# Performance work log

Hardware: AMD Instinct MI355X
Metric: run time of the kernel (lower is better)

## Reference

```python
import jax, jax.numpy as jnp
import numpy as np

HEADS = 64
HEAD_DIM = 4
C = 256
T = 32  # num_ds_tokens
MAX_Q_CHUNK = 256


def conv1x1(x, W, b):
    # x: (N,C,H,W), W: (O,C), b: (O,)
    return jnp.einsum('oc,nchw->nohw', W, x) + b[None, :, None, None]


def reshape_heads(x):
    n, c, h, w = x.shape
    return x.reshape(n, HEADS, HEAD_DIM, h * w)


def chunked_attention(q, k, v, ds_token_count, chunk):
    # q: (N,h,d,L); k,v: (N,h,d,M)
    N, H, D, L = q.shape
    scale = 1.0 / float(np.sqrt(D))
    nc = L // chunk
    qs = q.reshape(N, H, D, nc, chunk).transpose(3, 0, 1, 2, 4)  # (nc,N,h,d,chunk)

    def body(carry, qc):
        logits = jnp.einsum('nhdl,nhdm->nhlm', qc, k) * scale
        w = jax.nn.softmax(logits, axis=-1)
        out = jnp.einsum('nhlm,nhdm->nhdl', w, v)
        total = jnp.clip(w.sum(axis=-1, keepdims=True), 1e-6, None)
        dsr = w[..., -ds_token_count:].sum(axis=-1, keepdims=True) / total  # (N,h,chunk,1)
        return carry, (out, dsr)

    _, (outs, dsrs) = jax.lax.scan(body, None, qs)
    attn_out = outs.transpose(1, 2, 3, 0, 4).reshape(N, H, D, L)
    ds_ratio_mean = dsrs.mean(axis=(0, 2, 3, 4))  # mean over heads, tokens -> (N,)
    return attn_out, ds_ratio_mean


def forward(spatials, invs, dss, Wq, bq, Wk, bk, Wv, bv, Wo, bo, Wdsk, bdsk, Wdsv, bdsv, ds_gate):
    fused_feats = []
    ds_ratios = []
    for i in range(4):
        sp, inv, ds = spatials[i], invs[i], dss[i]
        N, c, Hh, Ww = sp.shape
        q = reshape_heads(conv1x1(sp, Wq[i], bq[i]))
        k_sp = reshape_heads(conv1x1(inv, Wk[i], bk[i]))
        v_sp = reshape_heads(conv1x1(inv, Wv[i], bv[i]))
        pooled = ds.mean(axis=(2, 3))  # (N,C)
        key_tok = (pooled @ Wdsk[i].T + bdsk[i]).reshape(N, HEADS, HEAD_DIM, T)
        val_tok = (pooled @ Wdsv[i].T + bdsv[i]).reshape(N, HEADS, HEAD_DIM, T)
        gate = jax.nn.sigmoid(ds_gate[i])
        val_tok = val_tok * gate
        k = jnp.concatenate([k_sp, key_tok], axis=-1)
        v = jnp.concatenate([v_sp, val_tok], axis=-1)
        L = Hh * Ww
        chunk = min(MAX_Q_CHUNK, L)
        attn_out, dsr = chunked_attention(q, k, v, T, chunk)
        attn_out = attn_out.reshape(N, C, Hh, Ww)
        fused = sp + conv1x1(attn_out, Wo[i], bo[i])
        fused_feats.append(fused)
        ds_ratios.append(dsr)
    return (*fused_feats, jnp.stack(ds_ratios))


def setup_inputs() -> dict:
    key = jax.random.key(0)
    ks = jax.random.split(key, 32)
    sizes = [64, 32, 16, 8]
    inp = {}
    j = 0
    for pref in ('s', 'i', 'd'):
        for lvl, hw in enumerate(sizes):
            inp[f'{pref}{lvl}'] = jax.random.normal(ks[j], (2, C, hw, hw), dtype=jnp.float32)
            j += 1
    w = 0.02
    inp['Wq'] = jax.random.normal(ks[j], (4, C, C), dtype=jnp.float32) * w; j += 1
    inp['bq'] = jnp.zeros((4, C), dtype=jnp.float32)
    inp['Wk'] = jax.random.normal(ks[j], (4, C, C), dtype=jnp.float32) * w; j += 1
    inp['bk'] = jnp.zeros((4, C), dtype=jnp.float32)
    inp['Wv'] = jax.random.normal(ks[j], (4, C, C), dtype=jnp.float32) * w; j += 1
    inp['bv'] = jnp.zeros((4, C), dtype=jnp.float32)
    inp['Wo'] = jax.random.normal(ks[j], (4, C, C), dtype=jnp.float32) * w; j += 1
    inp['bo'] = jnp.zeros((4, C), dtype=jnp.float32)
    inp['Wdsk'] = jax.random.normal(ks[j], (4, HEADS * HEAD_DIM * T, C), dtype=jnp.float32) * w; j += 1
    inp['bdsk'] = jnp.zeros((4, HEADS * HEAD_DIM * T), dtype=jnp.float32)
    inp['Wdsv'] = jax.random.normal(ks[j], (4, HEADS * HEAD_DIM * T, C), dtype=jnp.float32) * w; j += 1
    inp['bdsv'] = jnp.zeros((4, HEADS * HEAD_DIM * T), dtype=jnp.float32)
    inp['ds_gate'] = jnp.zeros((4,), dtype=jnp.float32)
    return inp


def reference(s0, s1, s2, s3, i0, i1, i2, i3, d0, d1, d2, d3,
              Wq, bq, Wk, bk, Wv, bv, Wo, bo, Wdsk, bdsk, Wdsv, bdsv, ds_gate):
    return forward((s0, s1, s2, s3), (i0, i1, i2, i3), (d0, d1, d2, d3),
                   Wq, bq, Wk, bk, Wv, bv, Wo, bo, Wdsk, bdsk, Wdsv, bdsv, ds_gate)
```

## Files before the change

kernel.cpp:

```cpp
#include <hip/hip_runtime.h>
#include <math.h>

#define CCH 256
#define NB 2
#define HEADS 64
#define QK_SCALE (0.72134752f * 1024.0f)
#define SCH_MAGIC 15316.0f

typedef _Float16 f16;
typedef _Float16 f16x8 __attribute__((ext_vector_type(8)));
typedef _Float16 f16x4 __attribute__((ext_vector_type(4)));
typedef float f32x4 __attribute__((ext_vector_type(4)));

static const size_t OFF_POOLED = 0;
static const size_t OFF_DSACC  = 2048;
static const size_t H_Q   = 0;
static const size_t H_K   = 2785280;
static const size_t H_V   = 5636096;
static const size_t H_ATT = 8486912;
static const size_t H_SPT = 11272192;
static const size_t H_IVT = 14057472;
static const size_t H_W   = 16842752;

static const size_t DS_OUT_OFF = 2785280;

__device__ __forceinline__ void lvl_tables(int lvl, int& L, int& M, size_t& qo, size_t& kvo) {
    const int Ls[4] = {4096, 1024, 256, 64};
    const size_t qoff[4] = {0, 2097152, 2621440, 2752512};
    const size_t kvoff[4] = {0, 2113536, 2654208, 2801664};
    L = Ls[lvl]; M = L + 32; qo = qoff[lvl]; kvo = kvoff[lvl];
}

struct P12 { const float* a[12]; };

__global__ __launch_bounds__(256)
void prep_kernel(P12 ptrs, const float* __restrict__ Wq, const float* __restrict__ Wk,
                 const float* __restrict__ Wv, const float* __restrict__ Wo,
                 f16* __restrict__ WF, f16* __restrict__ spT, f16* __restrict__ ivT,
                 float* __restrict__ pooled, float* __restrict__ dsacc) {
    int id = blockIdx.x;
    if (id < 5440) {
        __shared__ float tile[32][33];
        int x = id % 170, rest = id / 170;
        int y = rest & 7, z = rest >> 3;
        int lvl, xl;
        if (x < 128) { lvl = 0; xl = x; }
        else if (x < 160) { lvl = 1; xl = x - 128; }
        else if (x < 168) { lvl = 2; xl = x - 160; }
        else { lvl = 3; xl = x - 168; }
        int L, M; size_t qo, kvo;
        lvl_tables(lvl, L, M, qo, kvo);
        int src = z >> 1, n = z & 1;
        const float* X = ptrs.a[src * 4 + lvl];
        f16* XT = (src == 0 ? spT : ivT) + qo;
        int c0 = y * 32, l0 = xl * 32;
        int tx = threadIdx.x & 31, ty = threadIdx.x >> 5;
        #pragma unroll
        for (int k = 0; k < 4; k++) {
            int c = c0 + ty + k * 8;
            tile[ty + k * 8][tx] = X[((size_t)n * CCH + c) * L + l0 + tx];
        }
        __syncthreads();
        #pragma unroll
        for (int k = 0; k < 4; k++) {
            int l = l0 + ty + k * 8;
            XT[((size_t)n * L + l) * CCH + c0 + tx] = (f16)tile[tx][ty + k * 8];
        }
    } else if (id < 6464) {
        int wI = id - 5440;
        int x = wI & 255, setId = wI >> 8;
        const float* src = (setId == 0) ? Wq : (setId == 1) ? Wk : (setId == 2) ? Wv : Wo;
        size_t i = ((size_t)x * 256 + threadIdx.x) * 4;
        float4 v = *(const float4*)(src + i);
        f16x4 o;
        o[0] = (f16)v.x; o[1] = (f16)v.y; o[2] = (f16)v.z; o[3] = (f16)v.w;
        *(f16x4*)(WF + (size_t)setId * 262144 + i) = o;
    } else {
        if (id == 6464) {
            dsacc[threadIdx.x] = 0.f;
            dsacc[threadIdx.x + 256] = 0.f;
        }
        int lin = (id - 6464) * 4 + (threadIdx.x >> 6);
        int c = lin & 255, n = (lin >> 8) & 1, lvl = lin >> 9;
        int t = threadIdx.x & 63;
        const float* d = ptrs.a[8 + lvl];
        int L = 4096 >> (2 * lvl);
        const float* p = d + ((size_t)n * CCH + c) * L;
        float s = 0.f;
        for (int i = t; i < L; i += 64) s += p[i];
        #pragma unroll
        for (int off = 32; off > 0; off >>= 1) s += __shfl_down(s, off);
        if (t == 0) pooled[(lvl * NB + n) * CCH + c] = s / (float)L;
    }
}

__global__ __launch_bounds__(256)
void mid_kernel(const f16* __restrict__ spT, const f16* __restrict__ ivT,
                const f16* __restrict__ WF,
                const float* __restrict__ bq, const float* __restrict__ bk,
                const float* __restrict__ bv,
                f16* __restrict__ qF, f16* __restrict__ kF, f16* __restrict__ vF,
                const float* __restrict__ Wdsk, const float* __restrict__ bdsk,
                const float* __restrict__ Wdsv, const float* __restrict__ bdsv,
                const float* __restrict__ ds_gate, const float* __restrict__ pooled) {
    int id = blockIdx.x;
    if (id >= 1032) {
        int dI = id - 1032;
        int bx = dI & 63, lvl = dI >> 6;
        int t = threadIdx.x;
        int j = bx * 128 + (t >> 1);
        int half = t & 1;
        const float4* wk = (const float4*)(Wdsk + ((size_t)lvl * 8192 + j) * CCH) + half * 32;
        const float4* wv = (const float4*)(Wdsv + ((size_t)lvl * 8192 + j) * CCH) + half * 32;
        const float4* p0 = (const float4*)(pooled + (size_t)(lvl * NB + 0) * CCH) + half * 32;
        const float4* p1 = (const float4*)(pooled + (size_t)(lvl * NB + 1) * CCH) + half * 32;
        float ak0 = 0.f, ak1 = 0.f, av0 = 0.f, av1 = 0.f;
        #pragma unroll 8
        for (int c4 = 0; c4 < 32; c4++) {
            float4 a = wk[c4], b = wv[c4], pa = p0[c4], pb = p1[c4];
            ak0 += a.x * pa.x + a.y * pa.y + a.z * pa.z + a.w * pa.w;
            ak1 += a.x * pb.x + a.y * pb.y + a.z * pb.z + a.w * pb.w;
            av0 += b.x * pa.x + b.y * pa.y + b.z * pa.z + b.w * pa.w;
            av1 += b.x * pb.x + b.y * pb.y + b.z * pb.z + b.w * pb.w;
        }
        ak0 += __shfl_xor(ak0, 1); ak1 += __shfl_xor(ak1, 1);
        av0 += __shfl_xor(av0, 1); av1 += __shfl_xor(av1, 1);
        if (half) return;
        float bk_ = bdsk[lvl * 8192 + j], bv_ = bdsv[lvl * 8192 + j];
        float gate = 1.f / (1.f + __expf(-ds_gate[lvl]));
        ak0 += bk_; ak1 += bk_;
        av0 = (av0 + bv_) * gate; av1 = (av1 + bv_) * gate;
        int o = j >> 5, tk = j & 31;
        int L, M; size_t qo, kvo;
        lvl_tables(lvl, L, M, qo, kvo);
        int hh = o >> 2, dd = o & 3;
        kF[kvo + ((size_t)(0 * 64 + hh)) * (4 * (size_t)M) + (size_t)(L + tk) * 4 + dd] = (f16)ak0;
        kF[kvo + ((size_t)(1 * 64 + hh)) * (4 * (size_t)M) + (size_t)(L + tk) * 4 + dd] = (f16)ak1;
        vF[kvo + ((size_t)(0 * 64 + hh)) * (4 * (size_t)M) + (size_t)dd * M + (L + tk)] = (f16)av0;
        vF[kvo + ((size_t)(1 * 64 + hh)) * (4 * (size_t)M) + (size_t)dd * M + (L + tk)] = (f16)av1;
        return;
    }
    int x = id % 43, rest = id / 43;
    int yb = rest % 12, n = rest / 12;
    int lvl, xl;
    if (x < 32) { lvl = 0; xl = x; }
    else if (x < 40) { lvl = 1; xl = x - 32; }
    else if (x < 42) { lvl = 2; xl = x - 40; }
    else { lvl = 3; xl = x - 42; }
    int L, M; size_t qo, kvo;
    lvl_tables(lvl, L, M, qo, kvo);
    const int type = yb >> 2;
    const int ob = (yb & 3) * 64;
    const int t = threadIdx.x, w = t >> 6, lane = t & 63;
    const int quad = lane >> 4, n16 = lane & 15;
    const int l0w = xl * 128 + w * 32;
    if (l0w >= L) return;

    const f16* XT = ((type == 0) ? spT : ivT) + qo;
    const f16* Wf = WF + (size_t)type * 262144 + (size_t)lvl * 65536;
    const float* bias = ((type == 0) ? bq : (type == 1) ? bk : bv) + lvl * 256;

    f32x4 acc[4][2];
    #pragma unroll
    for (int f = 0; f < 4; f++)
        #pragma unroll
        for (int g = 0; g < 2; g++) { acc[f][g][0]=0.f; acc[f][g][1]=0.f; acc[f][g][2]=0.f; acc[f][g][3]=0.f; }

    const f16* xp = XT + ((size_t)n * L + l0w + n16) * CCH + quad * 8;
    const f16* wp = Wf + ((size_t)(ob + n16)) * CCH + quad * 8;

    #pragma unroll
    for (int c0 = 0; c0 < 256; c0 += 32) {
        f16x8 af[4], bf[2];
        #pragma unroll
        for (int f = 0; f < 4; f++) af[f] = *(const f16x8*)(wp + (size_t)f * 16 * CCH + c0);
        #pragma unroll
        for (int g = 0; g < 2; g++) bf[g] = *(const f16x8*)(xp + (size_t)g * 16 * CCH + c0);
        #pragma unroll
        for (int f = 0; f < 4; f++)
            #pragma unroll
            for (int g = 0; g < 2; g++)
                acc[f][g] = __builtin_amdgcn_mfma_f32_16x16x32_f16(af[f], bf[g], acc[f][g], 0, 0, 0);
    }

    #pragma unroll
    for (int f = 0; f < 4; f++) {
        #pragma unroll
        for (int g = 0; g < 2; g++) {
            int lloc = l0w + g * 16 + n16;
            float vals[4];
            #pragma unroll
            for (int r = 0; r < 4; r++)
                vals[r] = acc[f][g][r] + bias[ob + f * 16 + quad * 4 + r];
            if (type == 0) {
                #pragma unroll
                for (int r = 0; r < 4; r++)
                    qF[qo + ((size_t)n * CCH + ob + f * 16 + quad * 4 + r) * (size_t)L + lloc] =
                        (f16)(vals[r] * QK_SCALE);
            } else if (type == 1) {
                f16x4 pk;
                #pragma unroll
                for (int r = 0; r < 4; r++) pk[r] = (f16)vals[r];
                int hh = (ob + f * 16 + quad * 4) >> 2;
                *(f16x4*)(kF + kvo + ((size_t)(n * 64 + hh)) * (4 * (size_t)M) + (size_t)lloc * 4) = pk;
            } else {
                int hh = (ob + f * 16 + quad * 4) >> 2;
                f16* vdst = vF + kvo + ((size_t)(n * 64 + hh)) * (4 * (size_t)M) + lloc;
                #pragma unroll
                for (int r = 0; r < 4; r++)
                    vdst[(size_t)r * M] = (f16)vals[r];
            }
        }
    }
}

__global__ __launch_bounds__(256, 6)
void attn_all_kernel(const f16* __restrict__ qBase, const f16* __restrict__ kBase,
                     const f16* __restrict__ vBase, f16* __restrict__ attBase,
                     float* __restrict__ dsacc) {
    int x = blockIdx.x, lvl, xl;
    if (x < 16) { lvl = 0; xl = x; }
    else if (x < 20) { lvl = 1; xl = x - 16; }
    else if (x < 21) { lvl = 2; xl = 0; }
    else { lvl = 3; xl = 0; }
    int L, M; size_t qo, kvo;
    lvl_tables(lvl, L, M, qo, kvo);
    const f16* qb = qBase + qo;
    f16* attT = attBase + qo;

    const int h = blockIdx.y, b = blockIdx.z;
    const int t = threadIdx.x, w = t >> 6, lane = t & 63;
    const int quad = lane >> 4, n16 = lane & 15;
    const size_t qbase = ((size_t)b * CCH + h * 4) * (size_t)L;
    const int mperm = ((n16 & 12) << 1) + (n16 & 3);
    const int base_tile = xl * 16;

    const f16* kh = kBase + kvo + ((size_t)(b * 64 + h)) * (4 * (size_t)M);
    const f16* vh = vBase + kvo + ((size_t)(b * 64 + h)) * (4 * (size_t)M);
    const f16* kpm = kh + (size_t)mperm * 4;
    const f16* vpm = vh + (size_t)(n16 & 3) * M + quad * 8;
    const bool vlane = (n16 < 4);

    f16x4 qf[4];
    f32x4 acc[4];
    #pragma unroll
    for (int i = 0; i < 4; i++) {
        #pragma unroll
        for (int e = 0; e < 4; e++) qf[i][e] = (f16)0.f;
        acc[i][0] = 0.f; acc[i][1] = 0.f; acc[i][2] = 0.f; acc[i][3] = 0.f;
    }

    f32x4 magic;
    magic[0] = SCH_MAGIC; magic[1] = SCH_MAGIC; magic[2] = SCH_MAGIC; magic[3] = SCH_MAGIC;

    f16x8 vcon0, vconL;
    {
        f16 c0 = (f16)((n16 == 4) ? 1.f : 0.f);
        f16 cL = (f16)((n16 == 4 || n16 == 5) ? 1.f : 0.f);
        #pragma unroll
        for (int e = 0; e < 8; e++) { vcon0[e] = c0; vconL[e] = cL; }
    }

#define LOADKV(m0_, ka_, kb_, vf_)                                                      \
    do {                                                                                \
        ka_ = *(const f16x4*)(kpm + (size_t)(m0_) * 4);                                 \
        kb_ = *(const f16x4*)(kpm + (size_t)(m0_) * 4 + 16);                            \
        vf_ = *(const f16x8*)(vpm + (m0_));                                             \
    } while (0)

#define COMPUTE32(ka_, kb_, vfl_, vcon_)                                                \
    do {                                                                                \
        f16x8 vf = vlane ? (vfl_) : (vcon_);                                            \
        f32x4 s[4][2];                                                                  \
        _Pragma("unroll")                                                               \
        for (int j = 0; j < 4; j++) {                                                   \
            s[j][0] = __builtin_amdgcn_mfma_f32_16x16x16f16((ka_), qf[j], magic, 0, 0, 0);  \
            s[j][1] = __builtin_amdgcn_mfma_f32_16x16x16f16((kb_), qf[j], magic, 0, 0, 0); \
        }                                                                               \
        _Pragma("unroll")                                                               \
        for (int j = 0; j < 4; j++) {                                                   \
            union { unsigned u[4]; f16x8 hh; } Wu;                                      \
            Wu.u[0] = ((unsigned)(int)s[j][0][0]) | (((unsigned)(int)s[j][0][1]) << 16); \
            Wu.u[1] = ((unsigned)(int)s[j][0][2]) | (((unsigned)(int)s[j][0][3]) << 16); \
            Wu.u[2] = ((unsigned)(int)s[j][1][0]) | (((unsigned)(int)s[j][1][1]) << 16); \
            Wu.u[3] = ((unsigned)(int)s[j][1][2]) | (((unsigned)(int)s[j][1][3]) << 16); \
            acc[j] = __builtin_amdgcn_mfma_f32_16x16x32_f16(Wu.hh, vf, acc[j], 0, 0, 0); \
        }                                                                               \
    } while (0)

    if (base_tile * 16 + 256 <= L) {
        if (quad == 0) {
            #pragma unroll
            for (int i = 0; i < 4; i++) {
                int l = (base_tile + i * 4 + w) * 16 + n16;
                #pragma unroll
                for (int d = 0; d < 4; d++) qf[i][d] = qb[qbase + (size_t)d * L + l];
            }
        }
        f16x4 kaA, kbA, kaB, kbB;
        f16x8 vA, vB;
        LOADKV(0, kaA, kbA, vA);
        for (int m0 = 0; m0 < L; m0 += 64) {
            LOADKV(m0 + 32, kaB, kbB, vB);
            COMPUTE32(kaA, kbA, vA, vcon0);
            LOADKV(m0 + 64, kaA, kbA, vA);
            COMPUTE32(kaB, kbB, vB, vcon0);
        }
        COMPUTE32(kaA, kbA, vA, vconL);
    } else {
        bool valid[4];
        #pragma unroll
        for (int i = 0; i < 4; i++) {
            int tl0 = (base_tile + i * 4 + w) * 16;
            valid[i] = (tl0 < L);
            if (valid[i] && quad == 0) {
                int l = tl0 + n16;
                #pragma unroll
                for (int d = 0; d < 4; d++) qf[i][d] = qb[qbase + (size_t)d * L + l];
            }
        }
        for (int m0 = 0; m0 < M; m0 += 32) {
            f16x4 ka = *(const f16x4*)(kpm + (size_t)m0 * 4);
            f16x4 kb2 = *(const f16x4*)(kpm + (size_t)m0 * 4 + 16);
            f16x8 vfl = *(const f16x8*)(vpm + m0);
            f16x8 vf = vlane ? vfl : ((m0 >= L) ? vconL : vcon0);
            f32x4 s[4][2];
            #pragma unroll
            for (int j = 0; j < 4; j++) {
                if (!valid[j]) continue;
                s[j][0] = __builtin_amdgcn_mfma_f32_16x16x16f16(ka, qf[j], magic, 0, 0, 0);
                s[j][1] = __builtin_amdgcn_mfma_f32_16x16x16f16(kb2, qf[j], magic, 0, 0, 0);
            }
            #pragma unroll
            for (int j = 0; j < 4; j++) {
                if (!valid[j]) continue;
                union { unsigned u[4]; f16x8 hh; } Wu;
                Wu.u[0] = ((unsigned)(int)s[j][0][0]) | (((unsigned)(int)s[j][0][1]) << 16);
                Wu.u[1] = ((unsigned)(int)s[j][0][2]) | (((unsigned)(int)s[j][0][3]) << 16);
                Wu.u[2] = ((unsigned)(int)s[j][1][0]) | (((unsigned)(int)s[j][1][1]) << 16);
                Wu.u[3] = ((unsigned)(int)s[j][1][2]) | (((unsigned)(int)s[j][1][3]) << 16);
                acc[j] = __builtin_amdgcn_mfma_f32_16x16x32_f16(Wu.hh, vf, acc[j], 0, 0, 0);
            }
        }
    }
#undef LOADKV
#undef COMPUTE32

    float dsr = 0.f;
    #pragma unroll
    for (int i = 0; i < 4; i++) {
        int tl0 = (base_tile + i * 4 + w) * 16;
        if (tl0 >= L) continue;
        #pragma unroll
        for (int r = 0; r < 4; r++) {
            float den = __shfl(acc[i][r], (lane & 48) | 4, 64);
            float rcp = 1.f / den;
            int l = tl0 + quad * 4 + r;
            if (n16 < 4)
                attT[((size_t)b * L + l) * CCH + h * 4 + n16] = (f16)(acc[i][r] * rcp);
            if (n16 == 5) dsr += acc[i][r] * rcp;
        }
    }
    dsr += __shfl_xor(dsr, 16, 64);
    dsr += __shfl_xor(dsr, 32, 64);
    if (n16 == 5 && quad == 0) atomicAdd(dsacc + (size_t)lvl * 128 + (size_t)b * 64 + h, dsr);
}

__global__ __launch_bounds__(256)
void convo_kernel(const f16* __restrict__ attT, const f16* __restrict__ WF,
                  const float* __restrict__ bo, const float* __restrict__ s0,
                  const float* __restrict__ s1, const float* __restrict__ s2,
                  const float* __restrict__ s3, float* __restrict__ out,
                  const float* __restrict__ dsacc) {
    if (blockIdx.x == 0 && blockIdx.y == 0 && blockIdx.z == 0 && threadIdx.x < 64) {
        int tt = threadIdx.x;
        #pragma unroll
        for (int i = 0; i < 8; i++) {
            float v = dsacc[i * 64 + tt];
            #pragma unroll
            for (int off = 32; off > 0; off >>= 1) v += __shfl_down(v, off);
            if (tt == 0) {
                int lv = i >> 1;
                out[DS_OUT_OFF + i] = v / (float)(HEADS * (4096 >> (2 * lv)));
            }
        }
    }
    int x = blockIdx.x, lvl, xl;
    if (x < 32) { lvl = 0; xl = x; }
    else if (x < 40) { lvl = 1; xl = x - 32; }
    else if (x < 42) { lvl = 2; xl = x - 40; }
    else { lvl = 3; xl = x - 42; }
    int L, M; size_t qo, kvo;
    lvl_tables(lvl, L, M, qo, kvo);
    const float* resid = (lvl == 0) ? s0 : (lvl == 1) ? s1 : (lvl == 2) ? s2 : s3;
    const int ob = blockIdx.y * 64;
    const int n = blockIdx.z;
    const int t = threadIdx.x, w = t >> 6, lane = t & 63;
    const int quad = lane >> 4, n16 = lane & 15;
    const int l0w = xl * 128 + w * 32;
    if (l0w >= L) return;

    const f16* Wf = WF + 3 * 262144 + (size_t)lvl * 65536;
    const float* bias = bo + lvl * 256;

    f32x4 acc[4][2];
    #pragma unroll
    for (int f = 0; f < 4; f++)
        #pragma unroll
        for (int g = 0; g < 2; g++) { acc[f][g][0]=0.f; acc[f][g][1]=0.f; acc[f][g][2]=0.f; acc[f][g][3]=0.f; }

    const f16* xp = attT + qo + ((size_t)n * L + l0w + n16) * CCH + quad * 8;
    const f16* wp = Wf + ((size_t)(ob + n16)) * CCH + quad * 8;

    #pragma unroll
    for (int c0 = 0; c0 < 256; c0 += 32) {
        f16x8 af[4], bf[2];
        #pragma unroll
        for (int f = 0; f < 4; f++) af[f] = *(const f16x8*)(wp + (size_t)f * 16 * CCH + c0);
        #pragma unroll
        for (int g = 0; g < 2; g++) bf[g] = *(const f16x8*)(xp + (size_t)g * 16 * CCH + c0);
        #pragma unroll
        for (int f = 0; f < 4; f++)
            #pragma unroll
            for (int g = 0; g < 2; g++)
                acc[f][g] = __builtin_amdgcn_mfma_f32_16x16x32_f16(af[f], bf[g], acc[f][g], 0, 0, 0);
    }

    #pragma unroll
    for (int f = 0; f < 4; f++) {
        #pragma unroll
        for (int g = 0; g < 2; g++) {
            int lloc = l0w + g * 16 + n16;
            #pragma unroll
            for (int r = 0; r < 4; r++) {
                size_t idx = qo + ((size_t)n * CCH + ob + f * 16 + quad * 4 + r) * (size_t)L + lloc;
                out[idx] = acc[f][g][r] + bias[ob + f * 16 + quad * 4 + r] + resid[idx - qo];
            }
        }
    }
}

extern "C" void kernel_launch(void* const* d_in, const int* in_sizes, int n_in,
                              void* d_out, int out_size, void* d_ws, size_t ws_size,
                              hipStream_t stream) {
    const float* sp[4] = {(const float*)d_in[0], (const float*)d_in[1], (const float*)d_in[2], (const float*)d_in[3]};
    const float* iv[4] = {(const float*)d_in[4], (const float*)d_in[5], (const float*)d_in[6], (const float*)d_in[7]};
    const float* dd[4] = {(const float*)d_in[8], (const float*)d_in[9], (const float*)d_in[10], (const float*)d_in[11]};
    const float* Wq = (const float*)d_in[12];
    const float* bq = (const float*)d_in[13];
    const float* Wk = (const float*)d_in[14];
    const float* bk = (const float*)d_in[15];
    const float* Wv = (const float*)d_in[16];
    const float* bv = (const float*)d_in[17];
    const float* Wo = (const float*)d_in[18];
    const float* bo = (const float*)d_in[19];
    const float* Wdsk = (const float*)d_in[20];
    const float* bdsk = (const float*)d_in[21];
    const float* Wdsv = (const float*)d_in[22];
    const float* bdsv = (const float*)d_in[23];
    const float* gate = (const float*)d_in[24];

    float* ws = (float*)d_ws;
    float* pooled = ws + OFF_POOLED;
    float* dsacc = ws + OFF_DSACC;
    f16* hb = (f16*)((char*)d_ws + 10240);
    f16* qF   = hb + H_Q;
    f16* kF   = hb + H_K;
    f16* vF   = hb + H_V;
    f16* attF = hb + H_ATT;
    f16* spT  = hb + H_SPT;
    f16* ivT  = hb + H_IVT;
    f16* WF   = hb + H_W;
    float* out = (float*)d_out;

    P12 ptrs;
    for (int i = 0; i < 4; i++) { ptrs.a[i] = sp[i]; ptrs.a[4 + i] = iv[i]; ptrs.a[8 + i] = dd[i]; }

    prep_kernel<<<dim3(6976), 256, 0, stream>>>(ptrs, Wq, Wk, Wv, Wo, WF, spT, ivT, pooled, dsacc);

    mid_kernel<<<dim3(1288), 256, 0, stream>>>(spT, ivT, WF, bq, bk, bv, qF, kF, vF,
                                               Wdsk, bdsk, Wdsv, bdsv, gate, pooled);

    attn_all_kernel<<<dim3(22, 64, 2), 256, 0, stream>>>(qF, kF, vF, attF, dsacc);

    convo_kernel<<<dim3(43, 4, 2), 256, 0, stream>>>(attF, WF, bo, sp[0], sp[1], sp[2], sp[3],
                                                     out, dsacc);
}
```

Before: 475.0 us.

## Interleave K layout for single 16-byte loads and deepen attention prefetch

Measured after the change: 900.4 us. 1.9x slower.

```diff
diff --git a/kernel.cpp b/kernel.cpp
--- a/kernel.cpp
+++ b/kernel.cpp
@@ -29,6 +29,11 @@
     const size_t qoff[4] = {0, 2097152, 2621440, 2752512};
     const size_t kvoff[4] = {0, 2113536, 2654208, 2801664};
     L = Ls[lvl]; M = L + 32; qo = qoff[lvl]; kvo = kvoff[lvl];
+}
+
+__device__ __forceinline__ size_t k_off(int l, int d) {
+    return ((size_t)(l >> 5)) * 128 + (size_t)((((l >> 3) & 3) * 4 + (l & 3)) * 8)
+         + (size_t)(((l >> 2) & 1) * 4) + (size_t)d;
 }
 
 struct P12 { const float* a[12]; };
@@ -134,8 +139,9 @@
         int L, M; size_t qo, kvo;
         lvl_tables(lvl, L, M, qo, kvo);
         int hh = o >> 2, dd = o & 3;
-        kF[kvo + ((size_t)(0 * 64 + hh)) * (4 * (size_t)M) + (size_t)(L + tk) * 4 + dd] = (f16)ak0;
-        kF[kvo + ((size_t)(1 * 64 + hh)) * (4 * (size_t)M) + (size_t)(L + tk) * 4 + dd] = (f16)ak1;
+        size_t koff = k_off(L + tk, dd);
+        kF[kvo + ((size_t)(0 * 64 + hh)) * (4 * (size_t)M) + koff] = (f16)ak0;
+        kF[kvo + ((size_t)(1 * 64 + hh)) * (4 * (size_t)M) + koff] = (f16)ak1;
         vF[kvo + ((size_t)(0 * 64 + hh)) * (4 * (size_t)M) + (size_t)dd * M + (L + tk)] = (f16)av0;
         vF[kvo + ((size_t)(1 * 64 + hh)) * (4 * (size_t)M) + (size_t)dd * M + (L + tk)] = (f16)av1;
         return;
@@ -201,8 +207,9 @@
                 f16x4 pk;
                 #pragma unroll
                 for (int r = 0; r < 4; r++) pk[r] = (f16)vals[r];
-                int hh = (ob + f * 16 + quad * 4) >> 2;
-                *(f16x4*)(kF + kvo + ((size_t)(n * 64 + hh)) * (4 * (size_t)M) + (size_t)lloc * 4) = pk;
+                int o4 = ob + f * 16 + quad * 4;
+                int hh = o4 >> 2;
+                *(f16x4*)(kF + kvo + ((size_t)(n * 64 + hh)) * (4 * (size_t)M) + k_off(lloc, 0)) = pk;
             } else {
                 int hh = (ob + f * 16 + quad * 4) >> 2;
                 f16* vdst = vF + kvo + ((size_t)(n * 64 + hh)) * (4 * (size_t)M) + lloc;
@@ -232,12 +239,11 @@
     const int t = threadIdx.x, w = t >> 6, lane = t & 63;
     const int quad = lane >> 4, n16 = lane & 15;
     const size_t qbase = ((size_t)b * CCH + h * 4) * (size_t)L;
-    const int mperm = ((n16 & 12) << 1) + (n16 & 3);
     const int base_tile = xl * 16;
 
     const f16* kh = kBase + kvo + ((size_t)(b * 64 + h)) * (4 * (size_t)M);
     const f16* vh = vBase + kvo + ((size_t)(b * 64 + h)) * (4 * (size_t)M);
-    const f16* kpm = kh + (size_t)mperm * 4;
+    const f16* kpmP = kh + n16 * 8;
     const f16* vpm = vh + (size_t)(n16 & 3) * M + quad * 8;
     const bool vlane = (n16 < 4);
 
@@ -261,21 +267,23 @@
         for (int e = 0; e < 8; e++) { vcon0[e] = c0; vconL[e] = cL; }
     }
 
-#define LOADKV(m0_, ka_, kb_, vf_)                                                      \
+#define LOADKV(m0_, kk_, vf_)                                                           \
     do {                                                                                \
-        ka_ = *(const f16x4*)(kpm + (size_t)(m0_) * 4);                                 \
-        kb_ = *(const f16x4*)(kpm + (size_t)(m0_) * 4 + 16);                            \
+        kk_ = *(const f16x8*)(kpmP + (size_t)(m0_) * 4);                                \
         vf_ = *(const f16x8*)(vpm + (m0_));                                             \
     } while (0)
 
-#define COMPUTE32(ka_, kb_, vfl_, vcon_)                                                \
+#define COMPUTE32(kk_, vfl_, vcon_)                                                     \
     do {                                                                                \
+        f16x4 ka = __builtin_shufflevector((kk_), (kk_), 0, 1, 2, 3);                   \
+        f16x4 kb2 = __builtin_shufflevector((kk_), (kk_), 4, 5, 6, 7);                  \
         f16x8 vf = vlane ? (vfl_) : (vcon_);                                            \
         f32x4 s[4][2];                                                                  \
+        __builtin_amdgcn_s_setprio(1);                                                  \
         _Pragma("unroll")                                                               \
         for (int j = 0; j < 4; j++) {                                                   \
-            s[j][0] = __builtin_amdgcn_mfma_f32_16x16x16f16((ka_), qf[j], magic, 0, 0, 0);  \
-            s[j][1] = __builtin_amdgcn_mfma_f32_16x16x16f16((kb_), qf[j], magic, 0, 0, 0); \
+            s[j][0] = __builtin_amdgcn_mfma_f32_16x16x16f16(ka, qf[j], magic, 0, 0, 0);  \
+            s[j][1] = __builtin_amdgcn_mfma_f32_16x16x16f16(kb2, qf[j], magic, 0, 0, 0); \
         }                                                                               \
         _Pragma("unroll")                                                               \
         for (int j = 0; j < 4; j++) {                                                   \
@@ -286,6 +294,7 @@
             Wu.u[3] = ((unsigned)(int)s[j][1][2]) | (((unsigned)(int)s[j][1][3]) << 16); \
             acc[j] = __builtin_amdgcn_mfma_f32_16x16x32_f16(Wu.hh, vf, acc[j], 0, 0, 0); \
         }                                                                               \
+        __builtin_amdgcn_s_setprio(0);                                                  \
     } while (0)
 
     if (base_tile * 16 + 256 <= L) {
@@ -297,16 +306,20 @@
                 for (int d = 0; d < 4; d++) qf[i][d] = qb[qbase + (size_t)d * L + l];
             }
         }
-        f16x4 kaA, kbA, kaB, kbB;
-        f16x8 vA, vB;
-        LOADKV(0, kaA, kbA, vA);
-        for (int m0 = 0; m0 < L; m0 += 64) {
-            LOADKV(m0 + 32, kaB, kbB, vB);
-            COMPUTE32(kaA, kbA, vA, vcon0);
-            LOADKV(m0 + 64, kaA, kbA, vA);
-            COMPUTE32(kaB, kbB, vB, vcon0);
-        }
-        COMPUTE32(kaA, kbA, vA, vconL);
+        f16x8 k0, k0b, k1, k1b, v0, v0b, v1, v1b;
+        LOADKV(0, k0, v0); LOADKV(32, k0b, v0b);
+        LOADKV(64, k1, v1); LOADKV(96, k1b, v1b);
+        for (int m0 = 0; m0 < L; m0 += 128) {
+            COMPUTE32(k0, v0, vcon0);
+            COMPUTE32(k0b, v0b, vcon0);
+            LOADKV(m0 + 128, k0, v0);
+            LOADKV(m0 + 160, k0b, v0b);
+            COMPUTE32(k1, v1, vcon0);
+            COMPUTE32(k1b, v1b, vcon0);
+            LOADKV(m0 + 192, k1, v1);
+            LOADKV(m0 + 224, k1b, v1b);
+        }
+        COMPUTE32(k0, v0, vconL);
     } else {
         bool valid[4];
         #pragma unroll
@@ -320,8 +333,9 @@
             }
         }
         for (int m0 = 0; m0 < M; m0 += 32) {
-            f16x4 ka = *(const f16x4*)(kpm + (size_t)m0 * 4);
-            f16x4 kb2 = *(const f16x4*)(kpm + (size_t)m0 * 4 + 16);
+            f16x8 kk = *(const f16x8*)(kpmP + (size_t)m0 * 4);
+            f16x4 ka = __builtin_shufflevector(kk, kk, 0, 1, 2, 3);
+            f16x4 kb2 = __builtin_shufflevector(kk, kk, 4, 5, 6, 7);
             f16x8 vfl = *(const f16x8*)(vpm + m0);
             f16x8 vf = vlane ? vfl : ((m0 >= L) ? vconL : vcon0);
             f32x4 s[4][2];
```

## Split attention key range across waves and combine partial sums in shared memory

Applied to the files above, without the earlier changes.

Measured after the change: 1.029 ms. 2.17x slower.

```diff
diff --git a/kernel.cpp b/kernel.cpp
--- a/kernel.cpp
+++ b/kernel.cpp
@@ -219,9 +219,9 @@
                      const f16* __restrict__ vBase, f16* __restrict__ attBase,
                      float* __restrict__ dsacc) {
     int x = blockIdx.x, lvl, xl;
-    if (x < 16) { lvl = 0; xl = x; }
-    else if (x < 20) { lvl = 1; xl = x - 16; }
-    else if (x < 21) { lvl = 2; xl = 0; }
+    if (x < 64) { lvl = 0; xl = x; }
+    else if (x < 80) { lvl = 1; xl = x - 64; }
+    else if (x < 84) { lvl = 2; xl = x - 80; }
     else { lvl = 3; xl = 0; }
     int L, M; size_t qo, kvo;
     lvl_tables(lvl, L, M, qo, kvo);
@@ -233,7 +233,7 @@
     const int quad = lane >> 4, n16 = lane & 15;
     const size_t qbase = ((size_t)b * CCH + h * 4) * (size_t)L;
     const int mperm = ((n16 & 12) << 1) + (n16 & 3);
-    const int base_tile = xl * 16;
+    const int bt = xl * 4;
 
     const f16* kh = kBase + kvo + ((size_t)(b * 64 + h)) * (4 * (size_t)M);
     const f16* vh = vBase + kvo + ((size_t)(b * 64 + h)) * (4 * (size_t)M);
@@ -259,6 +259,15 @@
         f16 cL = (f16)((n16 == 4 || n16 == 5) ? 1.f : 0.f);
         #pragma unroll
         for (int e = 0; e < 8; e++) { vcon0[e] = c0; vconL[e] = cL; }
+    }
+
+    if (quad == 0) {
+        #pragma unroll
+        for (int i = 0; i < 4; i++) {
+            int l = (bt + i) * 16 + n16;
+            #pragma unroll
+            for (int d = 0; d < 4; d++) qf[i][d] = qb[qbase + (size_t)d * L + l];
+        }
     }
 
 #define LOADKV(m0_, ka_, kb_, vf_)                                                      \
@@ -272,6 +281,7 @@
     do {                                                                                \
         f16x8 vf = vlane ? (vfl_) : (vcon_);                                            \
         f32x4 s[4][2];                                                                  \
+        __builtin_amdgcn_s_setprio(1);                                                  \
         _Pragma("unroll")                                                               \
         for (int j = 0; j < 4; j++) {                                                   \
             s[j][0] = __builtin_amdgcn_mfma_f32_16x16x16f16((ka_), qf[j], magic, 0, 0, 0);  \
@@ -286,80 +296,55 @@
             Wu.u[3] = ((unsigned)(int)s[j][1][2]) | (((unsigned)(int)s[j][1][3]) << 16); \
             acc[j] = __builtin_amdgcn_mfma_f32_16x16x32_f16(Wu.hh, vf, acc[j], 0, 0, 0); \
         }                                                                               \
+        __builtin_amdgcn_s_setprio(0);                                                  \
     } while (0)
 
-    if (base_tile * 16 + 256 <= L) {
-        if (quad == 0) {
-            #pragma unroll
-            for (int i = 0; i < 4; i++) {
-                int l = (base_tile + i * 4 + w) * 16 + n16;
-                #pragma unroll
-                for (int d = 0; d < 4; d++) qf[i][d] = qb[qbase + (size_t)d * L + l];
-            }
-        }
+    const int nch = M >> 5;
+    const int cbase = nch >> 2, crem = nch & 3;
+    const int c0 = w * cbase + (w < crem ? w : crem);
+    const int c1 = c0 + cbase + (w < crem ? 1 : 0);
+    int m0 = c0 << 5;
+    const int mend = c1 << 5;
+
+    {
         f16x4 kaA, kbA, kaB, kbB;
         f16x8 vA, vB;
-        LOADKV(0, kaA, kbA, vA);
-        for (int m0 = 0; m0 < L; m0 += 64) {
+        LOADKV(m0, kaA, kbA, vA);
+        for (; m0 + 64 <= mend; m0 += 64) {
             LOADKV(m0 + 32, kaB, kbB, vB);
-            COMPUTE32(kaA, kbA, vA, vcon0);
+            COMPUTE32(kaA, kbA, vA, (m0 >= L) ? vconL : vcon0);
             LOADKV(m0 + 64, kaA, kbA, vA);
-            COMPUTE32(kaB, kbB, vB, vcon0);
-        }
-        COMPUTE32(kaA, kbA, vA, vconL);
-    } else {
-        bool valid[4];
-        #pragma unroll
-        for (int i = 0; i < 4; i++) {
-            int tl0 = (base_tile + i * 4 + w) * 16;
-            valid[i] = (tl0 < L);
-            if (valid[i] && quad == 0) {
-                int l = tl0 + n16;
-                #pragma unroll
-                for (int d = 0; d < 4; d++) qf[i][d] = qb[qbase + (size_t)d * L + l];
-            }
-        }
-        for (int m0 = 0; m0 < M; m0 += 32) {
-            f16x4 ka = *(const f16x4*)(kpm + (size_t)m0 * 4);
-            f16x4 kb2 = *(const f16x4*)(kpm + (size_t)m0 * 4 + 16);
-            f16x8 vfl = *(const f16x8*)(vpm + m0);
-            f16x8 vf = vlane ? vfl : ((m0 >= L) ? vconL : vcon0);
-            f32x4 s[4][2];
-            #pragma unroll
-            for (int j = 0; j < 4; j++) {
-                if (!valid[j]) continue;
-                s[j][0] = __builtin_amdgcn_mfma_f32_16x16x16f16(ka, qf[j], magic, 0, 0, 0);
-                s[j][1] = __builtin_amdgcn_mfma_f32_16x16x16f16(kb2, qf[j], magic, 0, 0, 0);
-            }
-            #pragma unroll
-            for (int j = 0; j < 4; j++) {
-                if (!valid[j]) continue;
-                union { unsigned u[4]; f16x8 hh; } Wu;
-                Wu.u[0] = ((unsigned)(int)s[j][0][0]) | (((unsigned)(int)s[j][0][1]) << 16);
-                Wu.u[1] = ((unsigned)(int)s[j][0][2]) | (((unsigned)(int)s[j][0][3]) << 16);
-                Wu.u[2] = ((unsigned)(int)s[j][1][0]) | (((unsigned)(int)s[j][1][1]) << 16);
-                Wu.u[3] = ((unsigned)(int)s[j][1][2]) | (((unsigned)(int)s[j][1][3]) << 16);
-                acc[j] = __builtin_amdgcn_mfma_f32_16x16x32_f16(Wu.hh, vf, acc[j], 0, 0, 0);
-            }
-        }
+            COMPUTE32(kaB, kbB, vB, (m0 + 32 >= L) ? vconL : vcon0);
+        }
+        if (m0 < mend)
+            COMPUTE32(kaA, kbA, vA, (m0 >= L) ? vconL : vcon0);
     }
 #undef LOADKV
 #undef COMPUTE32
 
+    __shared__ float comb[4][4][4][64];
+    #pragma unroll
+    for (int i = 0; i < 4; i++)
+        #pragma unroll
+        for (int r = 0; r < 4; r++)
+            comb[w][i][r][lane] = acc[i][r];
+    __syncthreads();
+
+    float a4[4];
+    #pragma unroll
+    for (int r = 0; r < 4; r++)
+        a4[r] = comb[0][w][r][lane] + comb[1][w][r][lane] + comb[2][w][r][lane] + comb[3][w][r][lane];
+
+    const int tl0 = (bt + w) * 16;
     float dsr = 0.f;
     #pragma unroll
-    for (int i = 0; i < 4; i++) {
-        int tl0 = (base_tile + i * 4 + w) * 16;
-        if (tl0 >= L) continue;
-        #pragma unroll
-        for (int r = 0; r < 4; r++) {
-            float den = __shfl(acc[i][r], (lane & 48) | 4, 64);
-            float rcp = 1.f / den;
-            int l = tl0 + quad * 4 + r;
-            if (n16 < 4)
-                attT[((size_t)b * L + l) * CCH + h * 4 + n16] = (f16)(acc[i][r] * rcp);
-            if (n16 == 5) dsr += acc[i][r] * rcp;
-        }
+    for (int r = 0; r < 4; r++) {
+        float den = __shfl(a4[r], (lane & 48) | 4, 64);
+        float rcp = 1.f / den;
+        int l = tl0 + quad * 4 + r;
+        if (n16 < 4)
+            attT[((size_t)b * L + l) * CCH + h * 4 + n16] = (f16)(a4[r] * rcp);
+        if (n16 == 5) dsr += a4[r] * rcp;
     }
     dsr += __shfl_xor(dsr, 16, 64);
     dsr += __shfl_xor(dsr, 32, 64);
@@ -481,7 +466,7 @@
     mid_kernel<<<dim3(1288), 256, 0, stream>>>(spT, ivT, WF, bq, bk, bv, qF, kF, vF,
                                                Wdsk, bdsk, Wdsv, bdsv, gate, pooled);
 
-    attn_all_kernel<<<dim3(22, 64, 2), 256, 0, stream>>>(qF, kF, vF, attF, dsacc);
+    attn_all_kernel<<<dim3(85, 64, 2), 256, 0, stream>>>(qF, kF, vF, attF, dsacc);
 
     convo_kernel<<<dim3(43, 4, 2), 256, 0, stream>>>(attF, WF, bo, sp[0], sp[1], sp[2], sp[3],
                                                      out, dsacc);
```
